# Kernel optimization log

Measured on AMD Instinct MI355X. Metric: run time of the kernel, lower is better.

The kernel has to match this reference:

```python
import jax, jax.numpy as jnp
import numpy as np

B, C, H, W = 8, 512, 64, 64
K = 19       # num classes (Cityscapes)
CT = 256     # transform channels


def _proj(x, w, g, b):
    # 1x1 conv (no bias) + folded eval-mode BatchNorm (per-channel scale g, bias b) + ReLU
    # x: [B,Cin,H,W], w: [Cout,Cin]
    y = jnp.einsum('bchw,oc->bohw', x, w)
    return jax.nn.relu(y * g[None, :, None, None] + b[None, :, None, None])


def setup_inputs() -> dict:
    key = jax.random.key(0)
    ks = jax.random.split(key, 12)
    s = lambda i, shape: jax.random.normal(ks[i], shape, jnp.float32) * 0.05
    ones = lambda n: jnp.ones((n,), jnp.float32)
    zeros = lambda n: jnp.zeros((n,), jnp.float32)
    return {
        'x': jax.random.normal(ks[0], (B, C, H, W), jnp.float32),
        'preds': jax.random.normal(ks[1], (B, K, H, W), jnp.float32),
        'feats_il': jax.random.normal(ks[2], (B, C, H, W), jnp.float32),
        # query_project: two 1x1 conv+BN+ReLU blocks
        'q_w1': s(3, (CT, C)), 'q_g1': ones(CT), 'q_b1': zeros(CT),
        'q_w2': s(4, (CT, CT)), 'q_g2': ones(CT), 'q_b2': zeros(CT),
        # key_project: two 1x1 conv+BN+ReLU blocks
        'k_w1': s(5, (CT, C)), 'k_g1': ones(CT), 'k_b1': zeros(CT),
        'k_w2': s(6, (CT, CT)), 'k_g2': ones(CT), 'k_b2': zeros(CT),
        # value_project: one 1x1 conv+BN+ReLU (value_out_norm=True)
        'v_w': s(7, (CT, C)), 'v_g': ones(CT), 'v_b': zeros(CT),
        # out_project: one 1x1 conv+BN+ReLU
        'o_w': s(8, (C, CT)), 'o_g': ones(C), 'o_b': zeros(C),
    }


def reference(x, preds, feats_il, q_w1, q_g1, q_b1, q_w2, q_g2, q_b2,
              k_w1, k_g1, k_b1, k_w2, k_g2, k_b2, v_w, v_g, v_b, o_w, o_g, o_b):
    b, c, h, w = x.shape
    k = preds.shape[1]
    hw = h * w
    feats = x.reshape(b, c, hw).transpose(0, 2, 1)        # [B,HW,C]
    logits = preds.reshape(b, k, hw).transpose(0, 2, 1)   # [B,HW,K]
    argmax = jnp.argmax(logits, axis=-1)                  # [B,HW]
    onehot = jax.nn.one_hot(argmax, k, dtype=x.dtype)     # [B,HW,K]
    NEG = jnp.asarray(-1e9, x.dtype)
    masked = jnp.where(onehot > 0, logits, NEG)
    # per-class softmax over the pixels assigned to that class
    wgt = jax.nn.softmax(masked, axis=1)                  # [B,HW,K]
    cls_feat = jnp.einsum('bpk,bpc->bkc', wgt, feats)     # [B,K,C]
    # scatter class descriptor back to every pixel of that class
    feats_sl = jnp.take_along_axis(cls_feat, argmax[:, :, None], axis=1)  # [B,HW,C]
    feats_sl = feats_sl.transpose(0, 2, 1).reshape(b, c, h, w)
    # SelfAttentionBlock: query from inputs, key/value from feats_sl
    q = _proj(_proj(x, q_w1, q_g1, q_b1), q_w2, q_g2, q_b2)
    kk = _proj(_proj(feats_sl, k_w1, k_g1, k_b1), k_w2, k_g2, k_b2)
    v = _proj(feats_sl, v_w, v_g, v_b)
    ct = q.shape[1]
    qf = q.reshape(b, ct, hw).transpose(0, 2, 1)          # [B,HW,CT]
    kf = kk.reshape(b, ct, hw)                            # [B,CT,HW]
    vf = v.reshape(b, ct, hw).transpose(0, 2, 1)          # [B,HW,CT]
    sim = jnp.einsum('bqc,bck->bqk', qf, kf) * (ct ** -0.5)
    attn = jax.nn.softmax(sim, axis=-1)
    ctx = jnp.einsum('bqk,bkc->bqc', attn, vf)            # [B,HW,CT]
    ctx = ctx.transpose(0, 2, 1).reshape(b, ct, h, w)
    return _proj(ctx, o_w, o_g, o_b)
```

## Files before the change

### kernel.cpp

```cpp
#include <hip/hip_runtime.h>
#include <math.h>

#define HW 4096
#define NB 8
#define NK 19
#define CIN 512
#define CTC 256

typedef __attribute__((ext_vector_type(8))) short short8;
typedef __attribute__((ext_vector_type(4))) float f32x4;

__device__ inline unsigned short f2bf(float x) {
  unsigned u = __float_as_uint(x);
  return (unsigned short)((u + 0x7fffu + ((u >> 16) & 1u)) >> 16);
}
__device__ inline float bf2f(unsigned short h) {
  return __uint_as_float(((unsigned)h) << 16);
}
__device__ inline void gload16(const void* g, void* l) {
  __builtin_amdgcn_global_load_lds(
      (const __attribute__((address_space(1))) void*)g,
      (__attribute__((address_space(3))) void*)l, 16, 0, 0);
}

__global__ __launch_bounds__(256) void wk1a(
    const float* __restrict__ w1, const float* __restrict__ w2,
    const float* __restrict__ wo, unsigned short* __restrict__ wb1,
    unsigned short* __restrict__ wb2, unsigned short* __restrict__ wbo,
    uint4* __restrict__ cls_feat_z, const float* __restrict__ preds,
    float* __restrict__ bestg, int* __restrict__ clsg,
    unsigned int* __restrict__ Mu_part, unsigned int* __restrict__ cnt_part) {
  __shared__ unsigned int Mw[NK];
  __shared__ unsigned int Cw[NK];
  int bx = blockIdx.x;
  int tid = threadIdx.x;
  if (bx < 320) {
    int gid = bx * 256 + tid;
    int i = gid * 4;
    const float* src;
    unsigned short* dst;
    int off;
    if (i < 131072) { src = w1; dst = wb1; off = i; }
    else if (i < 196608) { src = w2; dst = wb2; off = i - 131072; }
    else { src = wo; dst = wbo; off = i - 196608; }
    float4 v = *(const float4*)(src + off);
    dst[off + 0] = f2bf(v.x);
    dst[off + 1] = f2bf(v.y);
    dst[off + 2] = f2bf(v.z);
    dst[off + 3] = f2bf(v.w);
    uint4 z = {0u, 0u, 0u, 0u};
    for (int j = gid; j < 19456; j += 81920) cls_feat_z[j] = z;
  } else {
    int bq = bx - 320;
    int b = bq >> 4, pblk = bq & 15;
    if (tid < NK) { Mw[tid] = 0u; Cw[tid] = 0u; }
    __syncthreads();
    int p = pblk * 256 + tid;
    const float* pb = preds + (size_t)b * NK * HW;
    float best = pb[p];
    int bi = 0;
#pragma unroll
    for (int k = 1; k < NK; ++k) {
      float v = pb[k * HW + p];
      if (v > best) { best = v; bi = k; }
    }
    bestg[b * HW + p] = best;
    clsg[b * HW + p] = bi;
    unsigned fb = __float_as_uint(best);
    unsigned key = (fb & 0x80000000u) ? ~fb : (fb | 0x80000000u);
    atomicMax(&Mw[bi], key);
    atomicAdd(&Cw[bi], 1u);
    __syncthreads();
    if (tid < 32) {
      Mu_part[(b * 16 + pblk) * 32 + tid] = (tid < NK) ? Mw[tid] : 0u;
      cnt_part[(b * 16 + pblk) * 32 + tid] = (tid < NK) ? Cw[tid] : 0u;
    }
  }
}

__global__ __launch_bounds__(256) void k1b(
    float* __restrict__ bestg, const int* __restrict__ clsg,
    const unsigned int* __restrict__ Mu_part, float* __restrict__ Zf_part) {
  int b = blockIdx.y, pblk = blockIdx.x;
  int tid = threadIdx.x;
  __shared__ float Mf[NK];
  __shared__ float Zw[NK];
  if (tid < NK) {
    unsigned key = 0u;
#pragma unroll
    for (int j = 0; j < 16; ++j) {
      unsigned v = Mu_part[(b * 16 + j) * 32 + tid];
      key = (v > key) ? v : key;
    }
    float m = -1e30f;
    if (key) {
      unsigned fb = (key & 0x80000000u) ? (key & 0x7fffffffu) : ~key;
      m = __uint_as_float(fb);
    }
    Mf[tid] = m;
    Zw[tid] = 0.f;
  }
  __syncthreads();
  int p = pblk * 256 + tid;
  int c = clsg[b * HW + p];
  float e = expf(bestg[b * HW + p] - Mf[c]);
  bestg[b * HW + p] = e;
  atomicAdd(&Zw[c], e);
  __syncthreads();
  if (tid < 32) Zf_part[(b * 16 + pblk) * 32 + tid] = (tid < NK) ? Zw[tid] : 0.f;
}

__global__ __launch_bounds__(256) void xk2(
    const float* __restrict__ x, const float* __restrict__ eg,
    const int* __restrict__ clsg, const float* __restrict__ Zf_part,
    unsigned short* __restrict__ xT, float* __restrict__ cls_feat) {
  __shared__ float tile[64][65];
  __shared__ unsigned short Bs[32 * 516];
  __shared__ float Zl[NK];
  int b = blockIdx.z, c0 = blockIdx.y * 64, pbase = blockIdx.x * 512;
  int tid = threadIdx.x;
  int l = tid & 63, w = tid >> 6;
  if (tid < NK) {
    float s = 0.f;
#pragma unroll
    for (int j = 0; j < 16; ++j) s += Zf_part[(b * 16 + j) * 32 + tid];
    Zl[tid] = s;
  }
  {
    uint4 z = {0u, 0u, 0u, 0u};
    for (int i = tid; i < 2064; i += 256) ((uint4*)Bs)[i] = z;
  }
  __syncthreads();
  for (int i = tid; i < 512; i += 256) {
    int c = clsg[b * HW + pbase + i];
    Bs[c * 516 + i] = f2bf(eg[b * HW + pbase + i] / Zl[c]);
  }
  f32x4 acc[2];
  acc[0] = (f32x4){0.f, 0.f, 0.f, 0.f};
  acc[1] = (f32x4){0.f, 0.f, 0.f, 0.f};
  int cbase = w * 16;
  for (int s = 0; s < 8; ++s) {
    int ps = pbase + s * 64;
    __syncthreads();
#pragma unroll
    for (int r = 0; r < 4; ++r) {
      int cl = r * 16 + (tid >> 4);
      int pl = (tid & 15) * 4;
      float4 v = *(const float4*)&x[((size_t)b * CIN + c0 + cl) * HW + ps + pl];
      tile[cl][pl + 0] = v.x;
      tile[cl][pl + 1] = v.y;
      tile[cl][pl + 2] = v.z;
      tile[cl][pl + 3] = v.w;
    }
    __syncthreads();
#pragma unroll
    for (int j = 0; j < 16; ++j) {
      int ploc = j * 4 + w;
      xT[((size_t)b * HW + ps + ploc) * CIN + c0 + l] = f2bf(tile[l][ploc]);
    }
#pragma unroll
    for (int ch = 0; ch < 2; ++ch) {
      int pt = ch * 32 + (l >> 4) * 8;
      union { short8 v; unsigned short u[8]; } af;
      const float* tp = &tile[cbase + (l & 15)][pt];
#pragma unroll
      for (int j = 0; j < 8; ++j) af.u[j] = f2bf(tp[j]);
      int pg = s * 64 + pt;
#pragma unroll
      for (int mf = 0; mf < 2; ++mf) {
        short8 bf = *(const short8*)&Bs[(mf * 16 + (l & 15)) * 516 + pg];
        acc[mf] =
            __builtin_amdgcn_mfma_f32_16x16x32_bf16(af.v, bf, acc[mf], 0, 0, 0);
      }
    }
  }
#pragma unroll
  for (int mf = 0; mf < 2; ++mf) {
    int k = mf * 16 + (l & 15);
    if (k < NK) {
#pragma unroll
      for (int r = 0; r < 4; ++r) {
        int c = c0 + cbase + (l >> 4) * 4 + r;
        atomicAdd(&cls_feat[((size_t)b * NK + k) * CIN + c], acc[mf][r]);
      }
    }
  }
}

__global__ __launch_bounds__(256) void k3a(
    const float* __restrict__ cls_feat, const float* __restrict__ kw1,
    const float* __restrict__ kg1, const float* __restrict__ kb1,
    const float* __restrict__ vw, const float* __restrict__ vg,
    const float* __restrict__ vb, float* __restrict__ h1g,
    float* __restrict__ Vcls) {
  int bk = blockIdx.y;
  int b = bk / NK, kc = bk % NK;
  int q = blockIdx.x;
  __shared__ float cf[CIN];
  int tid = threadIdx.x;
  const float* row = cls_feat + (size_t)bk * CIN;
  for (int i = tid; i < CIN; i += 256) cf[i] = row[i];
  __syncthreads();
  int o = tid >> 1, half = tid & 1;
  int col = q * 64 + (o & 63);
  const float* w =
      (o < 64) ? &kw1[(size_t)col * CIN] : &vw[(size_t)col * CIN];
  int base = half * 256;
  float acc[4] = {0.f, 0.f, 0.f, 0.f};
#pragma unroll 8
  for (int i = 0; i < 64; ++i) {
    float4 w4 = *(const float4*)&w[base + i * 4];
    const float* c4 = &cf[base + i * 4];
    acc[i & 3] += w4.x * c4[0] + w4.y * c4[1] + w4.z * c4[2] + w4.w * c4[3];
  }
  float s = (acc[0] + acc[1]) + (acc[2] + acc[3]);
  s += __shfl_xor(s, 1);
  if (half == 0) {
    if (o < 64) {
      h1g[(size_t)bk * CTC + col] = fmaxf(s * kg1[col] + kb1[col], 0.f);
    } else {
      Vcls[((size_t)b * CTC + col) * NK + kc] =
          fmaxf(s * vg[col] + vb[col], 0.f);
    }
  }
}

__global__ __launch_bounds__(256) void k3b(
    const float* __restrict__ h1g, const float* __restrict__ kw2,
    const float* __restrict__ kg2, const float* __restrict__ kb2,
    unsigned short* __restrict__ KclsT) {
  int bk = blockIdx.y;
  int q = blockIdx.x;
  __shared__ float h1[CTC];
  int tid = threadIdx.x;
  const float* row = h1g + (size_t)bk * CTC;
  if (tid < CTC) h1[tid] = row[tid];
  __syncthreads();
  int o = tid >> 2, part = tid & 3;
  int col = q * 64 + o;
  const float* w = &kw2[(size_t)col * CTC + part * 64];
  const float* c = &h1[part * 64];
  float acc[4] = {0.f, 0.f, 0.f, 0.f};
#pragma unroll
  for (int i = 0; i < 16; ++i) {
    float4 w4 = *(const float4*)&w[i * 4];
    acc[i & 3] += w4.x * c[i * 4] + w4.y * c[i * 4 + 1] + w4.z * c[i * 4 + 2] +
                  w4.w * c[i * 4 + 3];
  }
  float s = (acc[0] + acc[1]) + (acc[2] + acc[3]);
  s += __shfl_xor(s, 1);
  s += __shfl_xor(s, 2);
  if (part == 0)
    KclsT[(size_t)bk * CTC + col] = f2bf(fmaxf(s * kg2[col] + kb2[col], 0.f));
}

template <int KD>
__global__ __launch_bounds__(256) void gemm_mfma(
    const unsigned short* __restrict__ A, const unsigned short* __restrict__ Wb,
    const float* __restrict__ g, const float* __restrict__ bb,
    void* __restrict__ Y, int M, int outmode) {
  __shared__ __align__(16) unsigned short As[2][128 * 32];
  __shared__ __align__(16) unsigned short Bs[2][128 * 32];
  int b = blockIdx.z;
  int n0 = blockIdx.x * 128;
  int m0 = blockIdx.y * 128;
  int tid = threadIdx.x;
  int l = tid & 63, wid = tid >> 6;
  int wr = wid >> 1, wc = wid & 1;
  const unsigned short* Ab = A + (size_t)b * HW * KD;

  f32x4 acc[4][4];
#pragma unroll
  for (int i = 0; i < 4; ++i)
#pragma unroll
    for (int j = 0; j < 4; ++j) acc[i][j] = (f32x4){0.f, 0.f, 0.f, 0.f};

  const int NT = KD / 32;
  auto STAGE = [&](int buf, int t) {
    int k0 = t * 32;
#pragma unroll
    for (int q = 0; q < 2; ++q) {
      int e = q * 2048 + tid * 8;
      int rl = e >> 5, sl = (e >> 3) & 3;
      gload16(Ab + (size_t)(n0 + rl) * KD + k0 + 8 * (sl ^ ((rl >> 1) & 3)),
              &As[buf][q * 2048 + wid * 512]);
    }
#pragma unroll
    for (int q = 0; q < 2; ++q) {
      int e = q * 2048 + tid * 8;
      int rl = e >> 5, sl = (e >> 3) & 3;
      gload16(Wb + (size_t)(m0 + rl) * KD + k0 + 8 * (sl ^ ((rl >> 1) & 3)),
              &Bs[buf][q * 2048 + wid * 512]);
    }
  };
  STAGE(0, 0);
  for (int t = 0; t < NT; ++t) {
    __syncthreads();
    if (t + 1 < NT) STAGE((t + 1) & 1, t + 1);
    int cur = t & 1;
    short8 af[4], bf[4];
#pragma unroll
    for (int f = 0; f < 4; ++f) {
      int nl = wr * 64 + f * 16 + (l & 15);
      af[f] = *(const short8*)&As[cur][nl * 32 + 8 * ((l >> 4) ^ ((nl >> 1) & 3))];
      int ml = wc * 64 + f * 16 + (l & 15);
      bf[f] = *(const short8*)&Bs[cur][ml * 32 + 8 * ((l >> 4) ^ ((ml >> 1) & 3))];
    }
#pragma unroll
    for (int i = 0; i < 4; ++i)
#pragma unroll
      for (int j = 0; j < 4; ++j)
        acc[i][j] =
            __builtin_amdgcn_mfma_f32_16x16x32_bf16(af[i], bf[j], acc[i][j], 0, 0, 0);
  }
  if (outmode == 0) {
    float* Yf = (float*)Y + (size_t)b * M * HW;
#pragma unroll
    for (int j = 0; j < 4; ++j) {
      int m = m0 + wc * 64 + j * 16 + (l & 15);
      float gm = g[m], bm = bb[m];
#pragma unroll
      for (int i = 0; i < 4; ++i) {
        int n = n0 + wr * 64 + i * 16 + (l >> 4) * 4;
        float4 o;
        o.x = fmaxf(acc[i][j][0] * gm + bm, 0.f);
        o.y = fmaxf(acc[i][j][1] * gm + bm, 0.f);
        o.z = fmaxf(acc[i][j][2] * gm + bm, 0.f);
        o.w = fmaxf(acc[i][j][3] * gm + bm, 0.f);
        *(float4*)&Yf[(size_t)m * HW + n] = o;
      }
    }
  } else {
    unsigned short* Yt = (unsigned short*)Y + (size_t)b * HW * M;
#pragma unroll
    for (int j = 0; j < 4; ++j) {
      int m = m0 + wc * 64 + j * 16 + (l & 15);
      float gm = g[m], bm = bb[m];
#pragma unroll
      for (int i = 0; i < 4; ++i) {
        int n = n0 + wr * 64 + i * 16 + (l >> 4) * 4;
#pragma unroll
        for (int r = 0; r < 4; ++r)
          Yt[(size_t)(n + r) * M + m] = f2bf(fmaxf(acc[i][j][r] * gm + bm, 0.f));
      }
    }
  }
}

__global__ __launch_bounds__(512, 1) void g1g2k5(
    const unsigned short* __restrict__ xT, const unsigned short* __restrict__ W1,
    const float* __restrict__ g1, const float* __restrict__ b1,
    const unsigned short* __restrict__ W2, const float* __restrict__ g2,
    const float* __restrict__ b2, const unsigned short* __restrict__ KclsT,
    const float* __restrict__ Vcls, const unsigned int* __restrict__ cnt_part,
    unsigned short* __restrict__ ctxT) {
  __shared__ __align__(16) char RC[49152];
  __shared__ __align__(16) unsigned short Q1f[8][4096];
  __shared__ __align__(16) unsigned short Kl2[32 * 32 * 8];
  __shared__ __align__(16) unsigned short Vl2[4 * 256 * 8];
  __shared__ float cntl[NK];
  unsigned short* As = (unsigned short*)RC;
  unsigned short* Bs = (unsigned short*)(RC + 16384);
  float* simT = (float*)RC;
  unsigned short* Pl = (unsigned short*)(RC + 16896);

  int b = blockIdx.y;
  int p0 = blockIdx.x * 128;
  int tid = threadIdx.x;
  int l = tid & 63, w = tid >> 6;
  int wp = w & 3, wm = w >> 2;
  const unsigned short* xTb = xT + ((size_t)b * HW + p0) * CIN;

  for (int i = tid; i < NK * 32; i += 512) {
    int m = i >> 5, s = i & 31;
    short8 v = *(const short8*)&KclsT[((size_t)b * NK + m) * CTC + s * 8];
    *(short8*)&Kl2[(s * 32 + m) * 8] = v;
  }
  for (int i = tid; i < 4 * 256; i += 512) {
    int s = i >> 8, c = i & 255;
    union { short8 v; unsigned short u[8]; } pk;
    const float* vr = &Vcls[((size_t)b * CTC + c) * NK];
#pragma unroll
    for (int j = 0; j < 8; ++j) {
      int k = s * 8 + j;
      pk.u[j] = (k < NK) ? f2bf(vr[k]) : (unsigned short)0;
    }
    *(short8*)&Vl2[(s * 256 + c) * 8] = pk.v;
  }
  if (tid < NK) {
    unsigned int s = 0u;
#pragma unroll
    for (int j = 0; j < 16; ++j) s += cnt_part[(b * 16 + j) * 32 + tid];
    cntl[tid] = (float)s;
  }

  f32x4 acc[2][8];

  auto STAGE_A1 = [&](int buf, int t) {
    int k0 = t * 32;
    int e = tid * 8;
    int rl = e >> 5, sl = (e >> 3) & 3;
    gload16(xTb + (size_t)rl * CIN + k0 + 8 * (sl ^ ((rl >> 1) & 3)),
            &As[buf * 4096 + w * 512]);
  };
  auto STAGE_B1 = [&](int buf, int t) {
    int k0 = t * 32;
#pragma unroll
    for (int q = 0; q < 2; ++q) {
      int e = q * 4096 + tid * 8;
      int rl = e >> 5, sl = (e >> 3) & 3;
      gload16(W1 + (size_t)rl * CIN + k0 + 8 * (sl ^ ((rl >> 1) & 3)),
              &Bs[buf * 8192 + q * 4096 + w * 512]);
    }
  };
#pragma unroll
  for (int i = 0; i < 2; ++i)
#pragma unroll
    for (int j = 0; j < 8; ++j) acc[i][j] = (f32x4){0.f, 0.f, 0.f, 0.f};
  STAGE_A1(0, 0);
  STAGE_B1(0, 0);
  for (int t = 0; t < 16; ++t) {
    __syncthreads();
    if (t + 1 < 16) { STAGE_A1((t + 1) & 1, t + 1); STAGE_B1((t + 1) & 1, t + 1); }
    int cur = t & 1;
    short8 af[2];
#pragma unroll
    for (int f = 0; f < 2; ++f) {
      int nl = wp * 32 + f * 16 + (l & 15);
      af[f] =
          *(const short8*)&As[cur * 4096 + nl * 32 + 8 * ((l >> 4) ^ ((nl >> 1) & 3))];
    }
#pragma unroll
    for (int mf = 0; mf < 8; ++mf) {
      int ml = wm * 128 + mf * 16 + (l & 15);
      short8 bf =
          *(const short8*)&Bs[cur * 8192 + ml * 32 + 8 * ((l >> 4) ^ ((ml >> 1) & 3))];
      acc[0][mf] =
          __builtin_amdgcn_mfma_f32_16x16x32_bf16(af[0], bf, acc[0][mf], 0, 0, 0);
      acc[1][mf] =
          __builtin_amdgcn_mfma_f32_16x16x32_bf16(af[1], bf, acc[1][mf], 0, 0, 0);
    }
  }
#pragma unroll
  for (int mf = 0; mf < 8; ++mf) {
    int ch = wm * 128 + mf * 16 + (l & 15);
    float gm = g1[ch], bm = b1[ch];
    int tq = ch >> 5, slot = (ch >> 3) & 3, wi = ch & 7;
#pragma unroll
    for (int i = 0; i < 2; ++i) {
#pragma unroll
      for (int r = 0; r < 4; ++r) {
        int p = wp * 32 + i * 16 + (l >> 4) * 4 + r;
        Q1f[tq][p * 32 + 8 * (slot ^ ((p >> 1) & 3)) + wi] =
            f2bf(fmaxf(acc[i][mf][r] * gm + bm, 0.f));
      }
    }
  }

  auto STAGE_B2 = [&](int buf, int t) {
    int k0 = t * 32;
#pragma unroll
    for (int q = 0; q < 2; ++q) {
      int e = q * 4096 + tid * 8;
      int rl = e >> 5, sl = (e >> 3) & 3;
      gload16(W2 + (size_t)rl * CTC + k0 + 8 * (sl ^ ((rl >> 1) & 3)),
              &Bs[buf * 8192 + q * 4096 + w * 512]);
    }
  };
#pragma unroll
  for (int i = 0; i < 2; ++i)
#pragma unroll
    for (int j = 0; j < 8; ++j) acc[i][j] = (f32x4){0.f, 0.f, 0.f, 0.f};
  STAGE_B2(0, 0);
  for (int t = 0; t < 8; ++t) {
    __syncthreads();
    if (t + 1 < 8) STAGE_B2((t + 1) & 1, t + 1);
    int cur = t & 1;
    short8 af[2];
#pragma unroll
    for (int f = 0; f < 2; ++f) {
      int nl = wp * 32 + f * 16 + (l & 15);
      af[f] = *(const short8*)&Q1f[t][nl * 32 + 8 * ((l >> 4) ^ ((nl >> 1) & 3))];
    }
#pragma unroll
    for (int mf = 0; mf < 8; ++mf) {
      int ml = wm * 128 + mf * 16 + (l & 15);
      short8 bf =
          *(const short8*)&Bs[cur * 8192 + ml * 32 + 8 * ((l >> 4) ^ ((ml >> 1) & 3))];
      acc[0][mf] =
          __builtin_amdgcn_mfma_f32_16x16x32_bf16(af[0], bf, acc[0][mf], 0, 0, 0);
      acc[1][mf] =
          __builtin_amdgcn_mfma_f32_16x16x32_bf16(af[1], bf, acc[1][mf], 0, 0, 0);
    }
  }
  __syncthreads();
#pragma unroll
  for (int mf = 0; mf < 8; ++mf) {
    int ch = wm * 128 + mf * 16 + (l & 15);
    float gm = g2[ch], bm = b2[ch];
    int tq = ch >> 5, slot = (ch >> 3) & 3, wi = ch & 7;
#pragma unroll
    for (int i = 0; i < 2; ++i) {
#pragma unroll
      for (int r = 0; r < 4; ++r) {
        int p = wp * 32 + i * 16 + (l >> 4) * 4 + r;
        Q1f[tq][p * 32 + 8 * (slot ^ ((p >> 1) & 3)) + wi] =
            f2bf(fmaxf(acc[i][mf][r] * gm + bm, 0.f));
      }
    }
  }
  __syncthreads();

  f32x4 a2[2];
  a2[0] = (f32x4){0.f, 0.f, 0.f, 0.f};
  a2[1] = (f32x4){0.f, 0.f, 0.f, 0.f};
  for (int t = 0; t < 8; ++t) {
    int nl = w * 16 + (l & 15);
    short8 aq =
        *(const short8*)&Q1f[t][nl * 32 + 8 * ((l >> 4) ^ ((nl >> 1) & 3))];
    int s = t * 4 + (l >> 4);
#pragma unroll
    for (int j = 0; j < 2; ++j) {
      int ml = j * 16 + (l & 15);
      short8 bk = *(const short8*)&Kl2[(s * 32 + ml) * 8];
      a2[j] = __builtin_amdgcn_mfma_f32_16x16x32_bf16(aq, bk, a2[j], 0, 0, 0);
    }
  }
  __syncthreads();
#pragma unroll
  for (int j = 0; j < 2; ++j) {
    int m = j * 16 + (l & 15);
    if (m < NK) {
#pragma unroll
      for (int r = 0; r < 4; ++r) {
        int p = w * 16 + (l >> 4) * 4 + r;
        simT[p * 33 + m] = a2[j][r];
      }
    }
  }
  __syncthreads();
  if (tid < 128) {
    float sims[NK];
#pragma unroll
    for (int k = 0; k < NK; ++k) sims[k] = simT[tid * 33 + k] * 0.0625f;
    float m = -1e30f;
#pragma unroll
    for (int k = 0; k < NK; ++k)
      if (cntl[k] > 0.f) m = fmaxf(m, sims[k]);
    float d = 0.f;
#pragma unroll
    for (int k = 0; k < NK; ++k) {
      float e = (cntl[k] > 0.f) ? expf(sims[k] - m) : 0.f;
      sims[k] = cntl[k] * e;
      d += sims[k];
    }
    float inv = 1.f / d;
#pragma unroll
    for (int s = 0; s < 4; ++s) {
      union { short8 v; unsigned short u8[8]; } pk;
#pragma unroll
      for (int j = 0; j < 8; ++j) {
        int k = s * 8 + j;
        pk.u8[j] = (k < NK) ? f2bf(sims[k] * inv) : (unsigned short)0;
      }
      *(short8*)&Pl[(s * 128 + tid) * 8] = pk.v;
    }
  }
  __syncthreads();
  short8 ap;
  {
    int nl = w * 16 + (l & 15);
    ap = *(const short8*)&Pl[((l >> 4) * 128 + nl) * 8];
  }
  unsigned short* cb = ctxT + ((size_t)b * HW + p0) * CTC;
#pragma unroll
  for (int mc = 0; mc < 4; ++mc) {
#pragma unroll
    for (int mf = 0; mf < 4; ++mf) {
      int ml = mc * 64 + mf * 16 + (l & 15);
      short8 bv = *(const short8*)&Vl2[((l >> 4) * 256 + ml) * 8];
      f32x4 z = {0.f, 0.f, 0.f, 0.f};
      f32x4 o = __builtin_amdgcn_mfma_f32_16x16x32_bf16(ap, bv, z, 0, 0, 0);
#pragma unroll
      for (int r = 0; r < 4; ++r) {
        int p = w * 16 + (l >> 4) * 4 + r;
        cb[(size_t)p * CTC + ml] = f2bf(o[r]);
      }
    }
  }
}

extern "C" void kernel_launch(void* const* d_in, const int* in_sizes, int n_in,
                              void* d_out, int out_size, void* d_ws, size_t ws_size,
                              hipStream_t stream) {
  const float* x = (const float*)d_in[0];
  const float* preds = (const float*)d_in[1];
  const float* q_w1 = (const float*)d_in[3];
  const float* q_g1 = (const float*)d_in[4];
  const float* q_b1 = (const float*)d_in[5];
  const float* q_w2 = (const float*)d_in[6];
  const float* q_g2 = (const float*)d_in[7];
  const float* q_b2 = (const float*)d_in[8];
  const float* k_w1 = (const float*)d_in[9];
  const float* k_g1 = (const float*)d_in[10];
  const float* k_b1 = (const float*)d_in[11];
  const float* k_w2 = (const float*)d_in[12];
  const float* k_g2 = (const float*)d_in[13];
  const float* k_b2 = (const float*)d_in[14];
  const float* v_w = (const float*)d_in[15];
  const float* v_g = (const float*)d_in[16];
  const float* v_b = (const float*)d_in[17];
  const float* o_w = (const float*)d_in[18];
  const float* o_g = (const float*)d_in[19];
  const float* o_b = (const float*)d_in[20];
  float* out = (float*)d_out;

  char* base = (char*)d_ws;
  unsigned short* xT = (unsigned short*)base;
  unsigned short* ctxT = (unsigned short*)(base + 33554432);
  char* f32r = base + 50331648;
  float* cls_feat = (float*)f32r;
  unsigned short* KclsT = (unsigned short*)(f32r + 311296);
  float* Vcls = (float*)(f32r + 389120);
  unsigned short* wb1 = (unsigned short*)(f32r + 544768);
  unsigned short* wb2 = (unsigned short*)(f32r + 806912);
  unsigned short* wbo = (unsigned short*)(f32r + 937984);
  float* h1g = (float*)(f32r + 1200128);
  float* bestg = (float*)(f32r + 1355776);
  int* clsg = (int*)(f32r + 1486848);
  unsigned int* Mu_part = (unsigned int*)(f32r + 1617920);
  unsigned int* cnt_part = (unsigned int*)(f32r + 1634304);
  float* Zf_part = (float*)(f32r + 1650688);

  wk1a<<<448, 256, 0, stream>>>(q_w1, q_w2, o_w, wb1, wb2, wbo,
                                (uint4*)cls_feat, preds, bestg, clsg, Mu_part,
                                cnt_part);
  k1b<<<dim3(16, NB), 256, 0, stream>>>(bestg, clsg, Mu_part, Zf_part);
  xk2<<<dim3(8, 8, NB), 256, 0, stream>>>(x, bestg, clsg, Zf_part, xT,
                                          cls_feat);
  k3a<<<dim3(4, NB * NK), 256, 0, stream>>>(cls_feat, k_w1, k_g1, k_b1, v_w,
                                            v_g, v_b, h1g, Vcls);
  k3b<<<dim3(4, NB * NK), 256, 0, stream>>>(h1g, k_w2, k_g2, k_b2, KclsT);
  g1g2k5<<<dim3(HW / 128, NB), 512, 0, stream>>>(xT, wb1, q_g1, q_b1, wb2,
                                                 q_g2, q_b2, KclsT, Vcls,
                                                 cnt_part, ctxT);
  gemm_mfma<CTC><<<dim3(32, 4, NB), 256, 0, stream>>>(ctxT, wbo, o_g, o_b,
                                                      (void*)out, CIN, 0);
}
```

Baseline: 119.1 us.

## Fuse output projection GEMM into attention kernel, dropping ctx round-trip

Folds the final 1x1 output projection (CT→C conv + BN + ReLU) into the fused query/attention kernel. The bf16 context tile now stays in shared memory (reusing the Q1f buffer with a swizzled layout), and each block streams output weights through LDS to produce its 128-pixel × 512-channel output directly. This removes one kernel launch and the global write and read of the ctxT intermediate. In exchange each block carries 128 extra accumulator registers at one block per CU, and the weight staging has no double buffering, so it syncs twice per k-step.

```diff
diff --git a/kernel.cpp b/kernel.cpp
--- a/kernel.cpp
+++ b/kernel.cpp
@@ -254,106 +254,14 @@
     KclsT[(size_t)bk * CTC + col] = f2bf(fmaxf(s * kg2[col] + kb2[col], 0.f));
 }
 
-template <int KD>
-__global__ __launch_bounds__(256) void gemm_mfma(
-    const unsigned short* __restrict__ A, const unsigned short* __restrict__ Wb,
-    const float* __restrict__ g, const float* __restrict__ bb,
-    void* __restrict__ Y, int M, int outmode) {
-  __shared__ __align__(16) unsigned short As[2][128 * 32];
-  __shared__ __align__(16) unsigned short Bs[2][128 * 32];
-  int b = blockIdx.z;
-  int n0 = blockIdx.x * 128;
-  int m0 = blockIdx.y * 128;
-  int tid = threadIdx.x;
-  int l = tid & 63, wid = tid >> 6;
-  int wr = wid >> 1, wc = wid & 1;
-  const unsigned short* Ab = A + (size_t)b * HW * KD;
-
-  f32x4 acc[4][4];
-#pragma unroll
-  for (int i = 0; i < 4; ++i)
-#pragma unroll
-    for (int j = 0; j < 4; ++j) acc[i][j] = (f32x4){0.f, 0.f, 0.f, 0.f};
-
-  const int NT = KD / 32;
-  auto STAGE = [&](int buf, int t) {
-    int k0 = t * 32;
-#pragma unroll
-    for (int q = 0; q < 2; ++q) {
-      int e = q * 2048 + tid * 8;
-      int rl = e >> 5, sl = (e >> 3) & 3;
-      gload16(Ab + (size_t)(n0 + rl) * KD + k0 + 8 * (sl ^ ((rl >> 1) & 3)),
-              &As[buf][q * 2048 + wid * 512]);
-    }
-#pragma unroll
-    for (int q = 0; q < 2; ++q) {
-      int e = q * 2048 + tid * 8;
-      int rl = e >> 5, sl = (e >> 3) & 3;
-      gload16(Wb + (size_t)(m0 + rl) * KD + k0 + 8 * (sl ^ ((rl >> 1) & 3)),
-              &Bs[buf][q * 2048 + wid * 512]);
-    }
-  };
-  STAGE(0, 0);
-  for (int t = 0; t < NT; ++t) {
-    __syncthreads();
-    if (t + 1 < NT) STAGE((t + 1) & 1, t + 1);
-    int cur = t & 1;
-    short8 af[4], bf[4];
-#pragma unroll
-    for (int f = 0; f < 4; ++f) {
-      int nl = wr * 64 + f * 16 + (l & 15);
-      af[f] = *(const short8*)&As[cur][nl * 32 + 8 * ((l >> 4) ^ ((nl >> 1) & 3))];
-      int ml = wc * 64 + f * 16 + (l & 15);
-      bf[f] = *(const short8*)&Bs[cur][ml * 32 + 8 * ((l >> 4) ^ ((ml >> 1) & 3))];
-    }
-#pragma unroll
-    for (int i = 0; i < 4; ++i)
-#pragma unroll
-      for (int j = 0; j < 4; ++j)
-        acc[i][j] =
-            __builtin_amdgcn_mfma_f32_16x16x32_bf16(af[i], bf[j], acc[i][j], 0, 0, 0);
-  }
-  if (outmode == 0) {
-    float* Yf = (float*)Y + (size_t)b * M * HW;
-#pragma unroll
-    for (int j = 0; j < 4; ++j) {
-      int m = m0 + wc * 64 + j * 16 + (l & 15);
-      float gm = g[m], bm = bb[m];
-#pragma unroll
-      for (int i = 0; i < 4; ++i) {
-        int n = n0 + wr * 64 + i * 16 + (l >> 4) * 4;
-        float4 o;
-        o.x = fmaxf(acc[i][j][0] * gm + bm, 0.f);
-        o.y = fmaxf(acc[i][j][1] * gm + bm, 0.f);
-        o.z = fmaxf(acc[i][j][2] * gm + bm, 0.f);
-        o.w = fmaxf(acc[i][j][3] * gm + bm, 0.f);
-        *(float4*)&Yf[(size_t)m * HW + n] = o;
-      }
-    }
-  } else {
-    unsigned short* Yt = (unsigned short*)Y + (size_t)b * HW * M;
-#pragma unroll
-    for (int j = 0; j < 4; ++j) {
-      int m = m0 + wc * 64 + j * 16 + (l & 15);
-      float gm = g[m], bm = bb[m];
-#pragma unroll
-      for (int i = 0; i < 4; ++i) {
-        int n = n0 + wr * 64 + i * 16 + (l >> 4) * 4;
-#pragma unroll
-        for (int r = 0; r < 4; ++r)
-          Yt[(size_t)(n + r) * M + m] = f2bf(fmaxf(acc[i][j][r] * gm + bm, 0.f));
-      }
-    }
-  }
-}
-
-__global__ __launch_bounds__(512, 1) void g1g2k5(
+__global__ __launch_bounds__(512, 1) void g1g2k5o(
     const unsigned short* __restrict__ xT, const unsigned short* __restrict__ W1,
     const float* __restrict__ g1, const float* __restrict__ b1,
     const unsigned short* __restrict__ W2, const float* __restrict__ g2,
     const float* __restrict__ b2, const unsigned short* __restrict__ KclsT,
     const float* __restrict__ Vcls, const unsigned int* __restrict__ cnt_part,
-    unsigned short* __restrict__ ctxT) {
+    const unsigned short* __restrict__ Wo, const float* __restrict__ og,
+    const float* __restrict__ ob, float* __restrict__ out) {
   __shared__ __align__(16) char RC[49152];
   __shared__ __align__(16) unsigned short Q1f[8][4096];
   __shared__ __align__(16) unsigned short Kl2[32 * 32 * 8];
@@ -363,6 +271,7 @@
   unsigned short* Bs = (unsigned short*)(RC + 16384);
   float* simT = (float*)RC;
   unsigned short* Pl = (unsigned short*)(RC + 16896);
+  unsigned short* WoBuf = (unsigned short*)RC;
 
   int b = blockIdx.y;
   int p0 = blockIdx.x * 128;
@@ -572,7 +481,6 @@
     int nl = w * 16 + (l & 15);
     ap = *(const short8*)&Pl[((l >> 4) * 128 + nl) * 8];
   }
-  unsigned short* cb = ctxT + ((size_t)b * HW + p0) * CTC;
 #pragma unroll
   for (int mc = 0; mc < 4; ++mc) {
 #pragma unroll
@@ -581,11 +489,61 @@
       short8 bv = *(const short8*)&Vl2[((l >> 4) * 256 + ml) * 8];
       f32x4 z = {0.f, 0.f, 0.f, 0.f};
       f32x4 o = __builtin_amdgcn_mfma_f32_16x16x32_bf16(ap, bv, z, 0, 0, 0);
+      int tq = ml >> 5, slot = (ml >> 3) & 3, wi = ml & 7;
 #pragma unroll
       for (int r = 0; r < 4; ++r) {
         int p = w * 16 + (l >> 4) * 4 + r;
-        cb[(size_t)p * CTC + ml] = f2bf(o[r]);
+        Q1f[tq][p * 32 + 8 * (slot ^ ((p >> 1) & 3)) + wi] = f2bf(o[r]);
       }
+    }
+  }
+
+  f32x4 a5[2][16];
+#pragma unroll
+  for (int i = 0; i < 2; ++i)
+#pragma unroll
+    for (int j = 0; j < 16; ++j) a5[i][j] = (f32x4){0.f, 0.f, 0.f, 0.f};
+  for (int t = 0; t < 8; ++t) {
+    __syncthreads();
+#pragma unroll
+    for (int q = 0; q < 4; ++q) {
+      int e = q * 4096 + tid * 8;
+      int rl = e >> 5, sl = (e >> 3) & 3;
+      gload16(Wo + (size_t)rl * CTC + t * 32 + 8 * (sl ^ ((rl >> 1) & 3)),
+              &WoBuf[q * 4096 + w * 512]);
+    }
+    __syncthreads();
+    short8 af[2];
+#pragma unroll
+    for (int f = 0; f < 2; ++f) {
+      int nl = wp * 32 + f * 16 + (l & 15);
+      af[f] = *(const short8*)&Q1f[t][nl * 32 + 8 * ((l >> 4) ^ ((nl >> 1) & 3))];
+    }
+#pragma unroll
+    for (int mf = 0; mf < 16; ++mf) {
+      int ml = wm * 256 + mf * 16 + (l & 15);
+      short8 bf =
+          *(const short8*)&WoBuf[ml * 32 + 8 * ((l >> 4) ^ ((ml >> 1) & 3))];
+      a5[0][mf] =
+          __builtin_amdgcn_mfma_f32_16x16x32_bf16(af[0], bf, a5[0][mf], 0, 0, 0);
+      a5[1][mf] =
+          __builtin_amdgcn_mfma_f32_16x16x32_bf16(af[1], bf, a5[1][mf], 0, 0, 0);
+    }
+  }
+  float* outb = out + (size_t)b * CIN * HW;
+#pragma unroll
+  for (int mf = 0; mf < 16; ++mf) {
+    int co = wm * 256 + mf * 16 + (l & 15);
+    float gm = og[co], bm = ob[co];
+#pragma unroll
+    for (int i = 0; i < 2; ++i) {
+      int n = p0 + wp * 32 + i * 16 + (l >> 4) * 4;
+      float4 o;
+      o.x = fmaxf(a5[i][mf][0] * gm + bm, 0.f);
+      o.y = fmaxf(a5[i][mf][1] * gm + bm, 0.f);
+      o.z = fmaxf(a5[i][mf][2] * gm + bm, 0.f);
+      o.w = fmaxf(a5[i][mf][3] * gm + bm, 0.f);
+      *(float4*)&outb[(size_t)co * HW + n] = o;
     }
   }
 }
@@ -617,8 +575,7 @@
 
   char* base = (char*)d_ws;
   unsigned short* xT = (unsigned short*)base;
-  unsigned short* ctxT = (unsigned short*)(base + 33554432);
-  char* f32r = base + 50331648;
+  char* f32r = base + 33554432;
   float* cls_feat = (float*)f32r;
   unsigned short* KclsT = (unsigned short*)(f32r + 311296);
   float* Vcls = (float*)(f32r + 389120);
@@ -641,9 +598,8 @@
   k3a<<<dim3(4, NB * NK), 256, 0, stream>>>(cls_feat, k_w1, k_g1, k_b1, v_w,
                                             v_g, v_b, h1g, Vcls);
   k3b<<<dim3(4, NB * NK), 256, 0, stream>>>(h1g, k_w2, k_g2, k_b2, KclsT);
-  g1g2k5<<<dim3(HW / 128, NB), 512, 0, stream>>>(xT, wb1, q_g1, q_b1, wb2,
-                                                 q_g2, q_b2, KclsT, Vcls,
-                                                 cnt_part, ctxT);
-  gemm_mfma<CTC><<<dim3(32, 4, NB), 256, 0, stream>>>(ctxT, wbo, o_g, o_b,
-                                                      (void*)out, CIN, 0);
-}
+  g1g2k5o<<<dim3(HW / 128, NB), 512, 0, stream>>>(xT, wb1, q_g1, q_b1, wb2,
+                                                  q_g2, q_b2, KclsT, Vcls,
+                                                  cnt_part, wbo, o_g, o_b,
+                                                  out);
+}
```

Result: faster. 113.3 us (-4.9%).
